# Performance work log

Measured on AMD Instinct MI355X. Metric: run time of the kernel, lower is better.

The kernel has to match this reference:

```python
import jax, jax.numpy as jnp
import numpy as np

MODEL_DIM = 512
NUM_HEADS = 8
HEAD_DIM = 64
INNER = NUM_HEADS * HEAD_DIM  # 512 == MODEL_DIM -> projection is Identity


def setup_inputs() -> dict:
    key = jax.random.key(0)
    ks = jax.random.split(key, 7)
    B, T = 2, 4096
    x = jax.random.normal(ks[0], (B, T, MODEL_DIM), dtype=jnp.float32)
    s = 1.0 / np.sqrt(MODEL_DIM)
    Wq = jax.random.normal(ks[1], (MODEL_DIM, INNER), dtype=jnp.float32) * s
    Wk = jax.random.normal(ks[2], (MODEL_DIM, INNER), dtype=jnp.float32) * s
    Wv = jax.random.normal(ks[3], (MODEL_DIM, INNER), dtype=jnp.float32) * s
    bq = jax.random.normal(ks[4], (INNER,), dtype=jnp.float32) * 0.01
    bk = jax.random.normal(ks[5], (INNER,), dtype=jnp.float32) * 0.01
    bv = jax.random.normal(ks[6], (INNER,), dtype=jnp.float32) * 0.01
    return {"x": x, "Wq": Wq, "bq": bq, "Wk": Wk, "bk": bk, "Wv": Wv, "bv": bv}


def reference(x, Wq, bq, Wk, bk, Wv, bv):
    B, T, _ = x.shape
    # project and split heads: [B, H, T, D]
    q = (x @ Wq + bq).reshape(B, T, NUM_HEADS, HEAD_DIM).transpose(0, 2, 1, 3)
    k = (x @ Wk + bk).reshape(B, T, NUM_HEADS, HEAD_DIM).transpose(0, 2, 1, 3)
    v = (x @ Wv + bv).reshape(B, T, NUM_HEADS, HEAD_DIM).transpose(0, 2, 1, 3)
    scale = 1.0 / np.sqrt(HEAD_DIM).astype(np.float32)
    attn = jnp.einsum('bhqd,bhkd->bhqk', q, k) * scale  # [B,H,Tq,Tkv]
    attn = jax.nn.softmax(attn, axis=-1)
    out = jnp.einsum('bhqk,bhkd->bhqd', attn, v)        # [B,H,Tq,D]
    out = out.transpose(0, 2, 1, 3).reshape(B, T, INNER)
    return out  # projection is Identity since INNER == MODEL_DIM
```

## Files before the change

### kernel.cpp

```cpp
#include <hip/hip_runtime.h>
#include <hip/hip_bf16.h>


typedef __attribute__((ext_vector_type(8)))  _Float16 half8;
typedef __attribute__((ext_vector_type(2)))  __fp16   fp16x2;
typedef __attribute__((ext_vector_type(4)))  float    f32x4;
typedef __attribute__((ext_vector_type(16))) float    f32x16;

#define TSEQ 4096
#define DH   64
#define NH   8
#define MD   512

#if __has_builtin(__builtin_amdgcn_exp2f)
__device__ inline float fexp2(float x){ return __builtin_amdgcn_exp2f(x); }
#else
__device__ inline float fexp2(float x){ float r; asm("v_exp_f32 %0, %1\n\ts_nop 1" : "=v"(r) : "v"(x)); return r; }
#endif

union H2U { fp16x2 h; unsigned int u; };
__device__ inline unsigned int pkrtz(float a, float b){
  H2U c; c.h = __builtin_amdgcn_cvt_pkrtz(a, b); return c.u;
}

__device__ inline void plswap(unsigned int &vdst, unsigned int &vsrc){
  asm volatile("v_permlane32_swap_b32 %0, %1" : "+v"(vdst), "+v"(vsrc));
}

union U4H8 { uint4 u; half8 h; };

#define AS3U(p) ((__attribute__((address_space(3))) unsigned int*)(p))
#define AS1U(p) ((const __attribute__((address_space(1))) unsigned int*)(p))

__global__ __launch_bounds__(256) void k_conv_x(const float* __restrict__ x, _Float16* __restrict__ xh){
  int i = (blockIdx.x*256 + threadIdx.x)*8;
  float4 a = *(const float4*)(x+i);
  float4 b = *(const float4*)(x+i+4);
  half8 o;
  o[0]=(_Float16)a.x; o[1]=(_Float16)a.y; o[2]=(_Float16)a.z; o[3]=(_Float16)a.w;
  o[4]=(_Float16)b.x; o[5]=(_Float16)b.y; o[6]=(_Float16)b.z; o[7]=(_Float16)b.w;
  *(half8*)(xh+i) = o;
}

__global__ __launch_bounds__(256) void k_prep_w(const float* __restrict__ Wq, const float* __restrict__ Wk,
                                                const float* __restrict__ Wv, _Float16* __restrict__ wt){
  __shared__ float tile[32][33];
  const int mat = blockIdx.z;
  const float* W = mat==0 ? Wq : (mat==1 ? Wk : Wv);
  const int n0 = blockIdx.x*32, k0 = blockIdx.y*32;
  const int tx = threadIdx.x & 31, ty = threadIdx.x >> 5;
  #pragma unroll
  for (int i=0;i<4;i++){ int k = ty*4+i; tile[k][tx] = W[(size_t)(k0+k)*MD + n0 + tx]; }
  __syncthreads();
  _Float16* dst = wt + (size_t)mat*MD*MD;
  #pragma unroll
  for (int i=0;i<4;i++){ int n = ty*4+i; dst[(size_t)(n0+n)*MD + k0 + tx] = (_Float16)tile[tx][n]; }
}

__global__ __launch_bounds__(256,2) void k_qkv(const _Float16* __restrict__ xh, const _Float16* __restrict__ wt,
              const float* __restrict__ bq, const float* __restrict__ bk, const float* __restrict__ bv,
              _Float16* __restrict__ qout, _Float16* __restrict__ kout, _Float16* __restrict__ vout){
  __shared__ alignas(16) _Float16 Ash[2][128*64];
  __shared__ alignas(16) _Float16 Bsh[2][128*64];
  const int tid = threadIdx.x, w = tid>>6, l = tid&63;
  const int fr = l&15, hi = l>>4;
  const int nt = blockIdx.x, mt = blockIdx.y;
  const int mat = nt>>2;
  const int n0  = (nt&3)*128;
  const int m0  = mt*128;
  const _Float16* W = wt + (size_t)mat*MD*MD;
  const int wr = (w>>1)*64, wc = (w&1)*64;

  f32x4 acc[4][4];
  #pragma unroll
  for (int a=0;a<4;a++)
    #pragma unroll
    for (int b=0;b<4;b++) acc[a][b] = (f32x4){0.f,0.f,0.f,0.f};

#define QSTAGE(k0_, buf) do { \
    _Pragma("unroll") \
    for (int i_=0;i_<4;i_++){ \
      int slot_ = tid + i_*256; \
      int row_ = slot_>>3, seg_ = (slot_&7) ^ (row_&7); \
      __builtin_amdgcn_global_load_lds(AS1U(xh + (size_t)(m0+row_)*MD + (k0_) + seg_*8), \
          AS3U((char*)&Ash[buf][0] + slot_*16), 16, 0, 0); \
      __builtin_amdgcn_global_load_lds(AS1U(W + (size_t)(n0+row_)*MD + (k0_) + seg_*8), \
          AS3U((char*)&Bsh[buf][0] + slot_*16), 16, 0, 0); \
    } \
  } while(0)

  QSTAGE(0, 0);

  for (int ks0=0; ks0<8; ks0++){
    const int cur = ks0&1;
    __syncthreads();
    if (ks0+1 < 8) QSTAGE((ks0+1)*64, cur^1);
    const _Float16* Ab = &Ash[cur][0];
    const _Float16* Bb = &Bsh[cur][0];
    #pragma unroll
    for (int ks=0;ks<2;ks++){
      half8 af[4], bfr[4];
      #pragma unroll
      for (int mi=0;mi<4;mi++){
        int row = wr + mi*16 + fr;
        af[mi] = *(const half8*)&Ab[row*64 + (((ks*4+hi) ^ (row&7))<<3)];
      }
      #pragma unroll
      for (int ni=0;ni<4;ni++){
        int row = wc + ni*16 + fr;
        bfr[ni] = *(const half8*)&Bb[row*64 + (((ks*4+hi) ^ (row&7))<<3)];
      }
      #pragma unroll
      for (int mi=0;mi<4;mi++)
        #pragma unroll
        for (int ni=0;ni<4;ni++)
          acc[mi][ni] = __builtin_amdgcn_mfma_f32_16x16x32_f16(af[mi], bfr[ni], acc[mi][ni], 0,0,0);
    }
  }
#undef QSTAGE

  const float* bias = mat==0 ? bq : (mat==1 ? bk : bv);
  const float scl = (mat==0) ? 0.125f*1.4426950408889634f : (mat==2 ? 0.0625f : 1.0f);
  if (mat==1){
    #pragma unroll
    for (int ni=0;ni<4;ni++){
      int n_in = n0 + wc + ni*16 + fr;
      float bb = bias[n_in];
      int h = n_in>>6, d = n_in&63;
      #pragma unroll
      for (int mi=0;mi<4;mi++)
        #pragma unroll
        for (int r=0;r<4;r++){
          int m = m0 + wr + mi*16 + hi*4 + r;
          float v = acc[mi][ni][r] + bb;
          int b_ = m>>12, t = m&4095;
          kout[ ((((size_t)(b_*NH + h))*8 + (d>>3))*TSEQ + t)*8 + (d&7) ] = (_Float16)v;
        }
    }
  } else {
    _Float16* dst = mat==0 ? qout : vout;
    #pragma unroll
    for (int ni=0;ni<4;ni++){
      int n_in = n0 + wc + ni*16 + fr;
      float bb = bias[n_in];
      int h = n_in>>6, d = n_in&63;
      #pragma unroll
      for (int mi=0;mi<4;mi++)
        #pragma unroll
        for (int r=0;r<4;r++){
          int m = m0 + wr + mi*16 + hi*4 + r;
          float v = (acc[mi][ni][r] + bb)*scl;
          int b_ = m>>12, t = m&4095;
          dst[ ((size_t)((b_*NH + h)*TSEQ + t))*DH + d ] = (_Float16)v;
        }
    }
  }
}

__global__ __launch_bounds__(256) void k_trans_v(const _Float16* __restrict__ v, _Float16* __restrict__ vtg){
  __shared__ _Float16 tile[64][72];
  const int tid = threadIdx.x;
  const int bh = blockIdx.y, t0 = blockIdx.x*64;
  const _Float16* src = v + ((size_t)bh*TSEQ + t0)*DH;
  #pragma unroll
  for (int i=0;i<2;i++){
    int slot = tid + i*256; int r = slot>>3, s = slot&7;
    *(half8*)&tile[r][s*8] = *(const half8*)(src + (size_t)r*DH + s*8);
  }
  __syncthreads();
  #pragma unroll
  for (int i=0;i<2;i++){
    int slot = tid + i*256;
    int d = slot&63, sg = slot>>6;
    half8 o;
    #pragma unroll
    for (int j=0;j<8;j++) o[j] = tile[sg*8+j][d];
    *(half8*)(vtg + (((size_t)bh*512 + (t0>>3) + sg)*64 + d)*8) = o;
  }
}

__global__ __launch_bounds__(256,2) void k_attn(const _Float16* __restrict__ qb_, const _Float16* __restrict__ ktg,
                                                const _Float16* __restrict__ vtg, float* __restrict__ out){
  __shared__ alignas(16) _Float16 Ksh[2*8192];
  __shared__ alignas(16) _Float16 Vsh[2*8192];
  const int tid = threadIdx.x, w = tid>>6, l = tid&63;
  const int ln31 = l&31, lh = l>>5;

  const int bid = blockIdx.x;
  const int swz = ((bid&7)<<6) | (bid>>3);
  const int bh = swz>>5, qblk = swz&31;

  const _Float16* Q  = qb_ + (size_t)bh*TSEQ*DH;
  const _Float16* Kt = ktg + (size_t)bh*8*TSEQ*8;
  const _Float16* Vt = vtg + (size_t)bh*512*64*8;
  const int q0 = qblk*128 + w*32;

  half8 qf[4];
  #pragma unroll
  for (int ds=0;ds<4;ds++)
    qf[ds] = *(const half8*)(Q + (size_t)(q0 + ln31)*DH + ds*16 + lh*8);

  f32x16 of0, of1, sacc;
  #pragma unroll
  for (int r=0;r<16;r++){ of0[r]=0.f; of1[r]=0.f; sacc[r]=0.f; }
  const half8 onesv = {(_Float16)1,(_Float16)1,(_Float16)1,(_Float16)1,
                       (_Float16)1,(_Float16)1,(_Float16)1,(_Float16)1};

  const int NT = TSEQ/128;
  const int kbase = lh*1024 + ln31*8;
  const int vbase = lh*512  + ln31*8;

#define STAGE(kt, buf) do { \
    const int k0_ = (kt)*128; \
    _Pragma("unroll") \
    for (int i_=0;i_<4;i_++){ \
      int base_ = i_*256 + w*64; \
      int slot_ = base_ + l; \
      int krow_ = slot_&127, kseg_ = slot_>>7; \
      __builtin_amdgcn_global_load_lds(AS1U(Kt + ((size_t)kseg_*TSEQ + k0_ + krow_)*8), \
          AS3U((char*)Ksh + (buf)*16384 + base_*16), 16, 0, 0); \
      __builtin_amdgcn_global_load_lds(AS1U(Vt + ((size_t)slot_ + k0_*8)*8), \
          AS3U((char*)Vsh + (buf)*16384 + base_*16), 16, 0, 0); \
    } \
  } while(0)

  STAGE(0, 0);

  for (int kt=0; kt<NT; kt++){
    const int cur = kt&1;
    __syncthreads();
    if (kt+1 < NT) STAGE(kt+1, cur^1);

    const _Float16* Kb = &Ksh[cur*8192];
    const _Float16* Vb = &Vsh[cur*8192];

    #pragma unroll
    for (int kbq=0; kbq<4; kbq++){
      f32x16 s;
      #pragma unroll
      for (int r=0;r<16;r++) s[r]=0.f;
      #pragma unroll
      for (int ds=0;ds<4;ds++){
        half8 kf = *(const half8*)&Kb[kbase + ds*2048 + kbq*256];
        s = __builtin_amdgcn_mfma_f32_32x32x16_f16(kf, qf[ds], s, 0,0,0);
      }

      unsigned int wv[8];
      #pragma unroll
      for (int c=0;c<4;c++){
        float e0 = fexp2(s[4*c+0]);
        float e1 = fexp2(s[4*c+1]);
        float e2 = fexp2(s[4*c+2]);
        float e3 = fexp2(s[4*c+3]);
        wv[2*c+0] = pkrtz(e0, e1);
        wv[2*c+1] = pkrtz(e2, e3);
      }

      #pragma unroll
      for (int e=0;e<2;e++){
        unsigned int a0 = wv[4*e+0], a1 = wv[4*e+1];
        unsigned int b0 = wv[4*e+2], b1 = wv[4*e+3];
        plswap(a0, b0);
        plswap(a1, b1);
        U4H8 pf; pf.u.x=a0; pf.u.y=a1; pf.u.z=b0; pf.u.w=b1;
        sacc = __builtin_amdgcn_mfma_f32_32x32x16_f16(onesv, pf.h, sacc, 0,0,0);
        half8 v0 = *(const half8*)&Vb[vbase + kbq*2048 + e*1024];
        half8 v1 = *(const half8*)&Vb[vbase + kbq*2048 + e*1024 + 256];
        of0 = __builtin_amdgcn_mfma_f32_32x32x16_f16(v0, pf.h, of0, 0,0,0);
        of1 = __builtin_amdgcn_mfma_f32_32x32x16_f16(v1, pf.h, of1, 0,0,0);
      }
    }
  }

  float inv = 16.0f / sacc[0];

  const int b_ = bh>>3, h = bh&7;
  float* o = out + ((size_t)(b_*TSEQ + q0 + ln31))*MD + h*DH;
  #pragma unroll
  for (int rr=0;rr<4;rr++){
    float4 o4 = { of0[4*rr+0]*inv, of0[4*rr+1]*inv, of0[4*rr+2]*inv, of0[4*rr+3]*inv };
    *(float4*)(o + rr*8 + lh*4) = o4;
  }
  #pragma unroll
  for (int rr=0;rr<4;rr++){
    float4 o4 = { of1[4*rr+0]*inv, of1[4*rr+1]*inv, of1[4*rr+2]*inv, of1[4*rr+3]*inv };
    *(float4*)(o + 32 + rr*8 + lh*4) = o4;
  }
#undef STAGE
}

extern "C" void kernel_launch(void* const* d_in, const int* in_sizes, int n_in,
                              void* d_out, int out_size, void* d_ws, size_t ws_size,
                              hipStream_t stream) {
  const float* x  = (const float*)d_in[0];
  const float* Wq = (const float*)d_in[1];
  const float* bq = (const float*)d_in[2];
  const float* Wk = (const float*)d_in[3];
  const float* bk = (const float*)d_in[4];
  const float* Wv = (const float*)d_in[5];
  const float* bv = (const float*)d_in[6];
  float* out = (float*)d_out;

  char* ws = (char*)d_ws;
  _Float16* xh = (_Float16*)(ws);
  _Float16* wt = (_Float16*)(ws + ((size_t)8<<20));
  _Float16* qb = (_Float16*)(ws + ((size_t)10<<20));
  _Float16* kb = (_Float16*)(ws + ((size_t)18<<20));
  _Float16* vb = (_Float16*)(ws + ((size_t)26<<20));
  _Float16* vt = xh;

  k_conv_x<<<2048, 256, 0, stream>>>(x, xh);
  k_prep_w<<<dim3(16,16,3), 256, 0, stream>>>(Wq, Wk, Wv, wt);
  k_qkv<<<dim3(12,64), 256, 0, stream>>>(xh, wt, bq, bk, bv, qb, kb, vb);
  k_trans_v<<<dim3(64,16), 256, 0, stream>>>(vb, vt);
  k_attn<<<512, 256, 0, stream>>>(qb, kb, vt, out);
}
```

Before: 133.8 us.

## Replace ones-MFMA row sum with VALU sum and batch two key blocks

The softmax denominator is now accumulated with VALU adds of the exp values plus one cross-half shuffle. This replaces the extra MFMA against a ones vector, which cost one in three of the PV-stage matrix instructions. The inner loop also handles two 32-key blocks per step and loads all of their K and V fragments from LDS up front, giving the scheduler more independent MFMAs and exps to interleave. The lane swap now uses the compiler builtin when available, so the compiler can schedule it. The cost is higher register pressure from the 16 preloaded fragments, and the row sum now uses fp32 exps instead of fp16-rounded ones.

```diff
diff --git a/kernel.cpp b/kernel.cpp
--- a/kernel.cpp
+++ b/kernel.cpp
@@ -6,6 +6,7 @@
 typedef __attribute__((ext_vector_type(2)))  __fp16   fp16x2;
 typedef __attribute__((ext_vector_type(4)))  float    f32x4;
 typedef __attribute__((ext_vector_type(16))) float    f32x16;
+typedef __attribute__((ext_vector_type(2)))  int      i32x2;
 
 #define TSEQ 4096
 #define DH   64
@@ -23,9 +24,16 @@
   H2U c; c.h = __builtin_amdgcn_cvt_pkrtz(a, b); return c.u;
 }
 
-__device__ inline void plswap(unsigned int &vdst, unsigned int &vsrc){
-  asm volatile("v_permlane32_swap_b32 %0, %1" : "+v"(vdst), "+v"(vsrc));
-}
+#if __has_builtin(__builtin_amdgcn_permlane32_swap)
+__device__ inline void plswap(unsigned int &a, unsigned int &b){
+  i32x2 r = __builtin_amdgcn_permlane32_swap((int)a, (int)b, false, false);
+  a = (unsigned int)r[0]; b = (unsigned int)r[1];
+}
+#else
+__device__ inline void plswap(unsigned int &a, unsigned int &b){
+  asm volatile("s_nop 1\n\tv_permlane32_swap_b32 %0, %1\n\ts_nop 1" : "+v"(a), "+v"(b));
+}
+#endif
 
 union U4H8 { uint4 u; half8 h; };
 
@@ -200,11 +208,10 @@
   for (int ds=0;ds<4;ds++)
     qf[ds] = *(const half8*)(Q + (size_t)(q0 + ln31)*DH + ds*16 + lh*8);
 
-  f32x16 of0, of1, sacc;
-  #pragma unroll
-  for (int r=0;r<16;r++){ of0[r]=0.f; of1[r]=0.f; sacc[r]=0.f; }
-  const half8 onesv = {(_Float16)1,(_Float16)1,(_Float16)1,(_Float16)1,
-                       (_Float16)1,(_Float16)1,(_Float16)1,(_Float16)1};
+  f32x16 of0, of1;
+  #pragma unroll
+  for (int r=0;r<16;r++){ of0[r]=0.f; of1[r]=0.f; }
+  float psum = 0.f;
 
   const int NT = TSEQ/128;
   const int kbase = lh*1024 + ln31*8;
@@ -235,44 +242,66 @@
     const _Float16* Vb = &Vsh[cur*8192];
 
     #pragma unroll
-    for (int kbq=0; kbq<4; kbq++){
-      f32x16 s;
-      #pragma unroll
-      for (int r=0;r<16;r++) s[r]=0.f;
+    for (int pair=0; pair<2; pair++){
+      half8 kf[8], vf[8];
       #pragma unroll
       for (int ds=0;ds<4;ds++){
-        half8 kf = *(const half8*)&Kb[kbase + ds*2048 + kbq*256];
-        s = __builtin_amdgcn_mfma_f32_32x32x16_f16(kf, qf[ds], s, 0,0,0);
-      }
-
-      unsigned int wv[8];
-      #pragma unroll
-      for (int c=0;c<4;c++){
-        float e0 = fexp2(s[4*c+0]);
-        float e1 = fexp2(s[4*c+1]);
-        float e2 = fexp2(s[4*c+2]);
-        float e3 = fexp2(s[4*c+3]);
-        wv[2*c+0] = pkrtz(e0, e1);
-        wv[2*c+1] = pkrtz(e2, e3);
-      }
-
-      #pragma unroll
-      for (int e=0;e<2;e++){
-        unsigned int a0 = wv[4*e+0], a1 = wv[4*e+1];
-        unsigned int b0 = wv[4*e+2], b1 = wv[4*e+3];
-        plswap(a0, b0);
-        plswap(a1, b1);
-        U4H8 pf; pf.u.x=a0; pf.u.y=a1; pf.u.z=b0; pf.u.w=b1;
-        sacc = __builtin_amdgcn_mfma_f32_32x32x16_f16(onesv, pf.h, sacc, 0,0,0);
-        half8 v0 = *(const half8*)&Vb[vbase + kbq*2048 + e*1024];
-        half8 v1 = *(const half8*)&Vb[vbase + kbq*2048 + e*1024 + 256];
-        of0 = __builtin_amdgcn_mfma_f32_32x32x16_f16(v0, pf.h, of0, 0,0,0);
-        of1 = __builtin_amdgcn_mfma_f32_32x32x16_f16(v1, pf.h, of1, 0,0,0);
+        kf[ds]   = *(const half8*)&Kb[kbase + ds*2048 + (pair*2+0)*256];
+        kf[4+ds] = *(const half8*)&Kb[kbase + ds*2048 + (pair*2+1)*256];
+      }
+      #pragma unroll
+      for (int ea=0;ea<4;ea++){
+        vf[2*ea]   = *(const half8*)&Vb[vbase + (pair*4+ea)*1024];
+        vf[2*ea+1] = *(const half8*)&Vb[vbase + (pair*4+ea)*1024 + 256];
+      }
+
+      f32x16 s0, s1;
+      #pragma unroll
+      for (int r=0;r<16;r++){ s0[r]=0.f; s1[r]=0.f; }
+      #pragma unroll
+      for (int ds=0;ds<4;ds++){
+        s0 = __builtin_amdgcn_mfma_f32_32x32x16_f16(kf[ds],   qf[ds], s0, 0,0,0);
+        s1 = __builtin_amdgcn_mfma_f32_32x32x16_f16(kf[4+ds], qf[ds], s1, 0,0,0);
+      }
+
+      unsigned int wv[16];
+      #pragma unroll
+      for (int m=0;m<2;m++){
+        #pragma unroll
+        for (int c=0;c<4;c++){
+          float v0_ = m ? s1[4*c+0] : s0[4*c+0];
+          float v1_ = m ? s1[4*c+1] : s0[4*c+1];
+          float v2_ = m ? s1[4*c+2] : s0[4*c+2];
+          float v3_ = m ? s1[4*c+3] : s0[4*c+3];
+          float e0 = fexp2(v0_);
+          float e1 = fexp2(v1_);
+          float e2 = fexp2(v2_);
+          float e3 = fexp2(v3_);
+          psum += (e0+e1)+(e2+e3);
+          wv[m*8+2*c+0] = pkrtz(e0, e1);
+          wv[m*8+2*c+1] = pkrtz(e2, e3);
+        }
+      }
+
+      #pragma unroll
+      for (int m=0;m<2;m++){
+        #pragma unroll
+        for (int e=0;e<2;e++){
+          unsigned int a0 = wv[m*8+4*e+0], a1 = wv[m*8+4*e+1];
+          unsigned int b0 = wv[m*8+4*e+2], b1 = wv[m*8+4*e+3];
+          plswap(a0, b0);
+          plswap(a1, b1);
+          U4H8 pf; pf.u.x=a0; pf.u.y=a1; pf.u.z=b0; pf.u.w=b1;
+          const int sl = m*2 + e;
+          of0 = __builtin_amdgcn_mfma_f32_32x32x16_f16(vf[2*sl],   pf.h, of0, 0,0,0);
+          of1 = __builtin_amdgcn_mfma_f32_32x32x16_f16(vf[2*sl+1], pf.h, of1, 0,0,0);
+        }
       }
     }
   }
 
-  float inv = 16.0f / sacc[0];
+  psum += __shfl_xor(psum, 32);
+  float inv = 16.0f / psum;
 
   const int b_ = bh>>3, h = bh&7;
   float* o = out + ((size_t)(b_*TSEQ + q0 + ln31))*MD + h*DH;
```

New measurement: 125.8 us. 1.06x faster.
